# Performance work log

Hardware: AMD Instinct MI355X
Metric: run time of the kernel (lower is better)

Reference implementation:

```python
import jax, jax.numpy as jnp
import numpy as np

# ---- architecture constants (from init_kwargs / arch_args) ----
IN_BITS, IN_FRAC, BITS_PER_STREAM = 8, 4, 2
N_STREAMS = IN_BITS // BITS_PER_STREAM          # 4
W_BITS, BITS_PER_SLICE = 8, 2
N_SLICES = W_BITS // BITS_PER_SLICE             # 4
ADC_BITS = 5
ADC_MAX = 2.0 ** ADC_BITS - 1.0                 # 31
SUBARRAY_SIZE = 128
IC, OC, K, STRIDE, PAD = 64, 64, 3, 1, 1
F_TOTAL = IC * K * K                            # 576 unfolded features
N_SUB = (F_TOTAL + SUBARRAY_SIZE - 1) // SUBARRAY_SIZE  # 5 subarrays
CHUNK = -(-F_TOTAL // N_SUB)                    # 116, matches torch.chunk sizes


def bit_stream(x):
    """VectorizedInputBitStreaming.forward: fixed-point quantize + two's complement + bit-serial split."""
    int_bits = IN_BITS - IN_FRAC - 1
    max_val = 2.0 ** int_bits - 2.0 ** (-IN_FRAC)
    q = jnp.round(jnp.clip(x, -(2.0 ** int_bits), max_val) * (2 ** IN_FRAC)).astype(jnp.int32)
    q = jnp.where(q < 0, (1 << IN_BITS) + q, q)  # two's complement encode
    shifts = jnp.arange(0, IN_BITS, BITS_PER_STREAM, dtype=jnp.int32)
    return ((q[..., None] >> shifts) & ((1 << BITS_PER_STREAM) - 1)).astype(jnp.float32)


def bit_slice(w):
    """VectorizedWeightBitSlicing.forward: pos/neg split, normalize by max abs, integer bit-slice."""
    wp = jnp.maximum(w, 0.0)
    wn = jnp.maximum(-w, 0.0)
    max_abs = jnp.maximum(wp.max(), wn.max())
    max_abs = jnp.where(max_abs > 0, max_abs, 1.0)
    mv = 2 ** W_BITS - 1
    pi = jnp.round(wp / max_abs * mv).astype(jnp.int32)
    ni = jnp.round(wn / max_abs * mv).astype(jnp.int32)
    shifts = jnp.arange(0, W_BITS, BITS_PER_SLICE, dtype=jnp.int32)
    mask = (1 << BITS_PER_SLICE) - 1
    pos = ((pi[..., None] >> shifts) & mask).astype(jnp.float32)
    neg = ((ni[..., None] >> shifts) & mask).astype(jnp.float32)
    return pos, neg, max_abs


def adc(x):
    """Nbit_ADC simulated: uniform round + clip to [0, 2^adc_bits - 1]."""
    return jnp.clip(jnp.round(x), 0.0, ADC_MAX)


def _forward(inputs, weight):
    # unfold -> (B, IC*K*K, H', W') with (c, kh, kw)-major feature ordering like F.unfold
    patches = jax.lax.conv_general_dilated_patches(
        inputs, (K, K), (STRIDE, STRIDE), [(PAD, PAD), (PAD, PAD)])
    B, F, H, W = patches.shape
    P = H * W
    patches = patches.reshape(B, F, P)

    streams = bit_stream(patches)                     # (B, F, P, S)
    pos_sl, neg_sl, norm = bit_slice(weight)
    pos_m = pos_sl.reshape(OC, F, N_SLICES)           # (O, F, T)
    neg_m = neg_sl.reshape(OC, F, N_SLICES)

    # zero-pad feature dim to N_SUB*CHUNK and reshape into subarray chunks
    pad = N_SUB * CHUNK - F
    streams = jnp.pad(streams, ((0, 0), (0, pad), (0, 0), (0, 0))).reshape(B, N_SUB, CHUNK, P, N_STREAMS)
    pos_m = jnp.pad(pos_m, ((0, 0), (0, pad), (0, 0))).reshape(OC, N_SUB, CHUNK, N_SLICES)
    neg_m = jnp.pad(neg_m, ((0, 0), (0, pad), (0, 0))).reshape(OC, N_SUB, CHUNK, N_SLICES)

    # per-subarray analog MAC: (c, b, o, p, s, t)
    pos_r = jnp.einsum('bcfps,ocft->cbopst', streams, pos_m)
    neg_r = jnp.einsum('bcfps,ocft->cbopst', streams, neg_m)

    # ADC quantize, then weight by 2^(stream*bits) * 2^(slice*bits), sum over s,t and subarrays c
    scale = (2.0 ** (jnp.arange(N_STREAMS) * BITS_PER_STREAM))[:, None] * \
            (2.0 ** (jnp.arange(N_SLICES) * BITS_PER_SLICE))[None, :]
    diff = jnp.einsum('cbopst,st->bop', adc(pos_r) - adc(neg_r), scale)

    out = diff * norm / (2.0 ** IN_BITS - 1.0)
    return out.reshape(B, OC, H, W), jnp.float32(0.0)


def setup_inputs() -> dict:
    key = jax.random.key(0)
    k1, k2 = jax.random.split(key)
    inputs = jax.random.normal(k1, (4, IC, 32, 32), dtype=jnp.float32)
    # kaiming_normal_-like init
    weight = jax.random.normal(k2, (OC, IC, K, K), dtype=jnp.float32) * (2.0 / (IC * K * K)) ** 0.5
    return {"inputs": inputs, "weight": weight}


def reference(inputs, weight):
    return _forward(inputs, weight)
```

## Files before the change

### kernel.cpp

```cpp
#include <hip/hip_runtime.h>
#include <stdint.h>


typedef int v4i __attribute__((ext_vector_type(4)));
typedef unsigned int v4u __attribute__((ext_vector_type(4)));

#define WS_PART   0
#define WS_AQ     1024
#define N_PART    144

__device__ __forceinline__ unsigned char quant_in(float x) {
  x = fminf(fmaxf(x, -8.0f), 7.9375f);
  int q = (int)rintf(x * 16.0f);
  return (unsigned char)(q & 255);
}

__global__ __launch_bounds__(256) void k_prep(
    const float* __restrict__ in, const float* __restrict__ w,
    unsigned char* __restrict__ Aq, float* __restrict__ part,
    float* __restrict__ out_scalar)
{
  int bid = blockIdx.x, tid = threadIdx.x;
  if (bid == 0 && tid == 0) out_scalar[0] = 0.0f;
  if (bid < 2560) {
    unsigned int widx = bid * 256 + tid;
    unsigned int m  = ((widx >> 5) * 52429u) >> 18;
    unsigned int kw = widx - m * 160;
    int b = m >> 10, p = m & 1023;
    int y = p >> 5, x = p & 31;
    unsigned int pack = 0;
    #pragma unroll
    for (int i = 0; i < 4; ++i) {
      unsigned int k = kw * 4 + i;
      unsigned int c = k >> 7;
      unsigned int j = k & 127;
      unsigned int csize = (c == 4) ? 112 : 116;
      unsigned int bv = 0;
      if (j < csize) {
        unsigned int f  = c * 116 + j;
        unsigned int ic = (f * 7282u) >> 16;
        unsigned int r9 = f - ic * 9;
        unsigned int dy = (r9 * 11u) >> 5;
        unsigned int dx = r9 - dy * 3;
        int iy = y + (int)dy - 1, ix = x + (int)dx - 1;
        if (iy >= 0 && iy < 32 && ix >= 0 && ix < 32)
          bv = quant_in(in[((b * 64 + ic) * 32 + iy) * 32 + ix]);
      }
      pack |= bv << (8 * i);
    }
    ((unsigned int*)Aq)[widx] = pack;
  } else {
    int t = (bid - 2560) * 256 + tid;
    const float4 wv = ((const float4*)w)[t];
    float a = fmaxf(fmaxf(fabsf(wv.x), fabsf(wv.y)),
                    fmaxf(fabsf(wv.z), fabsf(wv.w)));
    #pragma unroll
    for (int off = 32; off > 0; off >>= 1)
      a = fmaxf(a, __shfl_down(a, off, 64));
    if ((tid & 63) == 0)
      part[(bid - 2560) * 4 + (tid >> 6)] = a;
  }
}

__device__ __forceinline__ v4i bits2(v4u w, int s) {
  v4u r = (w >> (unsigned)(2 * s)) & 0x03030303u;
  return (v4i)r;
}

#define BROW 656

__global__ __launch_bounds__(256) void k_main(
    const unsigned char* __restrict__ Aq, const float* __restrict__ w,
    const float* __restrict__ part, float* __restrict__ out)
{
  __shared__ unsigned char Bl[2][16][BROW];
  __shared__ float s_norm;

  int tid   = threadIdx.x;
  int lane  = tid & 63;
  int wave  = tid >> 6;
  int mtile = blockIdx.x >> 2;
  int otile = blockIdx.x & 3;

  #pragma unroll
  for (int i = 0; i < 21; ++i) {
    int d = i * 256 + tid;
    if (d < 2 * 16 * BROW / 4) ((unsigned int*)Bl)[d] = 0u;
  }
  if (wave == 0) {
    float a = part[lane];
    a = fmaxf(a, part[lane + 64]);
    if (lane < 16) a = fmaxf(a, part[lane + 128]);
    #pragma unroll
    for (int off = 32; off > 0; off >>= 1)
      a = fmaxf(a, __shfl_down(a, off, 64));
    if (lane == 0) s_norm = (a > 0.0f) ? a : 1.0f;
  }
  __syncthreads();

  float norm = s_norm;
  float sc = 255.0f / norm;
  #pragma unroll
  for (int it = 0; it < 36; ++it) {
    int idx = it * 256 + tid;
    unsigned int ol = (((unsigned)idx >> 6) * 7282u) >> 16;
    unsigned int f  = idx - ol * 576;
    float wv = w[(otile * 16 + ol) * 576 + f];
    unsigned int c = (f * 565u) >> 16;
    unsigned int j = f - c * 116;
    int kpos = c * 128 + j;
    Bl[0][ol][kpos] = (unsigned char)(int)rintf(fmaxf(wv, 0.0f) * sc);
    Bl[1][ol][kpos] = (unsigned char)(int)rintf(fmaxf(-wv, 0.0f) * sc);
  }
  __syncthreads();

  int r16  = lane & 15;
  int kgrp = lane >> 4;
  int m = mtile * 64 + wave * 16 + r16;
  const unsigned char* ap = Aq + m * 640 + kgrp * 16;
  const unsigned char* bp = &Bl[0][r16][kgrp * 16];
  const unsigned char* bn = &Bl[1][r16][kgrp * 16];

  v4i outacc = {0, 0, 0, 0};

  #pragma unroll
  for (int c = 0; c < 5; ++c) {
    v4u a0 = *(const v4u*)(ap + c * 128);
    v4u a1 = *(const v4u*)(ap + c * 128 + 64);
    v4u p0 = *(const v4u*)(bp + c * 128);
    v4u p1 = *(const v4u*)(bp + c * 128 + 64);
    v4u n0 = *(const v4u*)(bn + c * 128);
    v4u n1 = *(const v4u*)(bn + c * 128 + 64);

    v4i btp0[4], btp1[4], btn0[4], btn1[4];
    #pragma unroll
    for (int t = 0; t < 4; ++t) {
      btp0[t] = bits2(p0, t); btp1[t] = bits2(p1, t);
      btn0[t] = bits2(n0, t); btn1[t] = bits2(n1, t);
    }

    #pragma unroll
    for (int s = 0; s < 4; ++s) {
      v4i as0 = bits2(a0, s), as1 = bits2(a1, s);
      #pragma unroll
      for (int t = 0; t < 4; ++t) {
        v4i z = {0, 0, 0, 0};
        v4i pacc = __builtin_amdgcn_mfma_i32_16x16x64_i8(as0, btp0[t], z, 0, 0, 0);
        pacc     = __builtin_amdgcn_mfma_i32_16x16x64_i8(as1, btp1[t], pacc, 0, 0, 0);
        v4i nacc = __builtin_amdgcn_mfma_i32_16x16x64_i8(as0, btn0[t], z, 0, 0, 0);
        nacc     = __builtin_amdgcn_mfma_i32_16x16x64_i8(as1, btn1[t], nacc, 0, 0, 0);
        int sh = 2 * (s + t);
        #pragma unroll
        for (int r = 0; r < 4; ++r) {
          int d = (pacc[r] < 31 ? pacc[r] : 31) - (nacc[r] < 31 ? nacc[r] : 31);
          outacc[r] += d << sh;
        }
      }
    }
  }

  float fsc = norm / 255.0f;
  int oc = otile * 16 + r16;
  #pragma unroll
  for (int r = 0; r < 4; ++r) {
    int mo = mtile * 64 + wave * 16 + kgrp * 4 + r;
    int b = mo >> 10, p = mo & 1023;
    out[(b * 64 + oc) * 1024 + p] = (float)outacc[r] * fsc;
  }
}

extern "C" void kernel_launch(void* const* d_in, const int* in_sizes, int n_in,
                              void* d_out, int out_size, void* d_ws, size_t ws_size,
                              hipStream_t stream) {
  const float* inp = (const float*)d_in[0];
  const float* wgt = (const float*)d_in[1];
  float* out = (float*)d_out;
  unsigned char* ws = (unsigned char*)d_ws;

  float*         part = (float*)(ws + WS_PART);
  unsigned char* Aq   = ws + WS_AQ;

  k_prep<<<2596, 256, 0, stream>>>(inp, wgt, Aq, part, out + 262144);
  k_main<<<256, 256, 0, stream>>>(Aq, wgt, part, out);
}
```

Baseline: 79.58 us.

## Fuse input quantization, weight max-reduce and MFMA into a single kernel

Merges the prep and main kernels into one launch. Each block quantizes its own 32-row patch tile into LDS, recomputes the global weight abs-max itself, and packs the weights with float4 loads. This removes the second launch and the global round trip of the quantized patch matrix. In exchange every block redundantly reads all the weights for the max, patch rows that straddle tiles are quantized more than once, and the tile shape changes to 32 pixels by 32 output channels, with MFMA operands swapped so stores go along the pixel dimension.

```diff
diff --git a/kernel.cpp b/kernel.cpp
--- a/kernel.cpp
+++ b/kernel.cpp
@@ -5,121 +5,127 @@
 typedef int v4i __attribute__((ext_vector_type(4)));
 typedef unsigned int v4u __attribute__((ext_vector_type(4)));
 
-#define WS_PART   0
-#define WS_AQ     1024
-#define N_PART    144
-
-__device__ __forceinline__ unsigned char quant_in(float x) {
-  x = fminf(fmaxf(x, -8.0f), 7.9375f);
-  int q = (int)rintf(x * 16.0f);
-  return (unsigned char)(q & 255);
-}
-
-__global__ __launch_bounds__(256) void k_prep(
-    const float* __restrict__ in, const float* __restrict__ w,
-    unsigned char* __restrict__ Aq, float* __restrict__ part,
-    float* __restrict__ out_scalar)
-{
-  int bid = blockIdx.x, tid = threadIdx.x;
-  if (bid == 0 && tid == 0) out_scalar[0] = 0.0f;
-  if (bid < 2560) {
-    unsigned int widx = bid * 256 + tid;
-    unsigned int m  = ((widx >> 5) * 52429u) >> 18;
-    unsigned int kw = widx - m * 160;
-    int b = m >> 10, p = m & 1023;
-    int y = p >> 5, x = p & 31;
-    unsigned int pack = 0;
-    #pragma unroll
-    for (int i = 0; i < 4; ++i) {
-      unsigned int k = kw * 4 + i;
-      unsigned int c = k >> 7;
-      unsigned int j = k & 127;
-      unsigned int csize = (c == 4) ? 112 : 116;
-      unsigned int bv = 0;
-      if (j < csize) {
-        unsigned int f  = c * 116 + j;
-        unsigned int ic = (f * 7282u) >> 16;
-        unsigned int r9 = f - ic * 9;
-        unsigned int dy = (r9 * 11u) >> 5;
-        unsigned int dx = r9 - dy * 3;
-        int iy = y + (int)dy - 1, ix = x + (int)dx - 1;
-        if (iy >= 0 && iy < 32 && ix >= 0 && ix < 32)
-          bv = quant_in(in[((b * 64 + ic) * 32 + iy) * 32 + ix]);
-      }
-      pack |= bv << (8 * i);
-    }
-    ((unsigned int*)Aq)[widx] = pack;
-  } else {
-    int t = (bid - 2560) * 256 + tid;
-    const float4 wv = ((const float4*)w)[t];
-    float a = fmaxf(fmaxf(fabsf(wv.x), fabsf(wv.y)),
-                    fmaxf(fabsf(wv.z), fabsf(wv.w)));
-    #pragma unroll
-    for (int off = 32; off > 0; off >>= 1)
-      a = fmaxf(a, __shfl_down(a, off, 64));
-    if ((tid & 63) == 0)
-      part[(bid - 2560) * 4 + (tid >> 6)] = a;
-  }
-}
+#define BROW 656
 
 __device__ __forceinline__ v4i bits2(v4u w, int s) {
   v4u r = (w >> (unsigned)(2 * s)) & 0x03030303u;
   return (v4i)r;
 }
 
-#define BROW 656
+__global__ __launch_bounds__(256) void k_fused(
+    const float* __restrict__ in, const float* __restrict__ w,
+    float* __restrict__ out)
+{
+  __shared__ unsigned char Al[32 * BROW];
+  __shared__ unsigned char Bl[64 * BROW];
+  __shared__ float s_part[4];
 
-__global__ __launch_bounds__(256) void k_main(
-    const unsigned char* __restrict__ Aq, const float* __restrict__ w,
-    const float* __restrict__ part, float* __restrict__ out)
-{
-  __shared__ unsigned char Bl[2][16][BROW];
-  __shared__ float s_norm;
+  int tid = threadIdx.x;
+  int bid = blockIdx.x;
+  if (bid == 0 && tid == 0) out[262144] = 0.0f;
 
-  int tid   = threadIdx.x;
-  int lane  = tid & 63;
-  int wave  = tid >> 6;
-  int mtile = blockIdx.x >> 2;
-  int otile = blockIdx.x & 3;
+  int mtile = bid >> 1;
+  int ohalf = bid & 1;
 
   #pragma unroll
-  for (int i = 0; i < 21; ++i) {
-    int d = i * 256 + tid;
-    if (d < 2 * 16 * BROW / 4) ((unsigned int*)Bl)[d] = 0u;
+  for (int i = 0; i < 5; ++i) {
+    int idx = i * 256 + tid;
+    int loc = idx >> 2, dw = idx & 3;
+    int sign = loc >= 160 ? 1 : 0;
+    int r = loc - sign * 160;
+    unsigned int o_l = ((unsigned)r * 52429u) >> 18;
+    int c = r - (int)o_l * 5;
+    ((unsigned int*)Bl)[(sign * 32 + (int)o_l) * 164 + c * 32 + 28 + dw] = 0u;
   }
-  if (wave == 0) {
-    float a = part[lane];
-    a = fmaxf(a, part[lane + 64]);
-    if (lane < 16) a = fmaxf(a, part[lane + 128]);
+
+  {
+    int b = mtile >> 5;
+    int pbase = (mtile & 31) * 32;
+    #pragma unroll 2
+    for (int i = 0; i < 20; ++i) {
+      int d = i * 256 + tid;
+      unsigned int m_l = ((unsigned)d * 52429u) >> 23;
+      int kw = d - (int)m_l * 160;
+      int p = pbase + (int)m_l;
+      int y = p >> 5, x = p & 31;
+      unsigned int pack = 0;
+      #pragma unroll
+      for (int q = 0; q < 4; ++q) {
+        int k = kw * 4 + q;
+        int c = k >> 7, j = k & 127;
+        int csize = (c == 4) ? 112 : 116;
+        unsigned int bv = 0;
+        if (j < csize) {
+          unsigned int f  = c * 116 + j;
+          unsigned int ic = (f * 7282u) >> 16;
+          unsigned int r9 = f - ic * 9u;
+          unsigned int dy = (r9 * 11u) >> 5;
+          unsigned int dx = r9 - dy * 3u;
+          int iy = y + (int)dy - 1, ix = x + (int)dx - 1;
+          if (iy >= 0 && iy < 32 && ix >= 0 && ix < 32) {
+            float xv = in[((b * 64 + (int)ic) * 32 + iy) * 32 + ix];
+            xv = fminf(fmaxf(xv, -8.0f), 7.9375f);
+            bv = (unsigned int)((int)rintf(xv * 16.0f) & 255);
+          }
+        }
+        pack |= bv << (8 * q);
+      }
+      ((unsigned int*)Al)[(int)m_l * 164 + kw] = pack;
+    }
+  }
+
+  {
+    const float4* w4 = (const float4*)w;
+    float a = 0.0f;
+    #pragma unroll 4
+    for (int i = 0; i < 36; ++i) {
+      float4 v = w4[i * 256 + tid];
+      a = fmaxf(a, fmaxf(fmaxf(fabsf(v.x), fabsf(v.y)),
+                         fmaxf(fabsf(v.z), fabsf(v.w))));
+    }
     #pragma unroll
     for (int off = 32; off > 0; off >>= 1)
       a = fmaxf(a, __shfl_down(a, off, 64));
-    if (lane == 0) s_norm = (a > 0.0f) ? a : 1.0f;
+    if ((tid & 63) == 0) s_part[tid >> 6] = a;
   }
   __syncthreads();
 
-  float norm = s_norm;
+  float norm = fmaxf(fmaxf(s_part[0], s_part[1]), fmaxf(s_part[2], s_part[3]));
+  if (!(norm > 0.0f)) norm = 1.0f;
   float sc = 255.0f / norm;
-  #pragma unroll
-  for (int it = 0; it < 36; ++it) {
-    int idx = it * 256 + tid;
-    unsigned int ol = (((unsigned)idx >> 6) * 7282u) >> 16;
-    unsigned int f  = idx - ol * 576;
-    float wv = w[(otile * 16 + ol) * 576 + f];
-    unsigned int c = (f * 565u) >> 16;
-    unsigned int j = f - c * 116;
-    int kpos = c * 128 + j;
-    Bl[0][ol][kpos] = (unsigned char)(int)rintf(fmaxf(wv, 0.0f) * sc);
-    Bl[1][ol][kpos] = (unsigned char)(int)rintf(fmaxf(-wv, 0.0f) * sc);
+
+  #pragma unroll 2
+  for (int i = 0; i < 18; ++i) {
+    int idx = i * 256 + tid;
+    unsigned int o_l = (((unsigned)idx >> 4) * 7282u) >> 16;
+    int g = idx - (int)o_l * 144;
+    int c, jg;
+    if (g < 116) { c = (g * 565) >> 14; jg = (g - c * 29) * 4; }
+    else         { c = 4;               jg = (g - 116) * 4; }
+    int f = c * 116 + jg;
+    float4 wv = *(const float4*)(w + (ohalf * 32 + (int)o_l) * 576 + f);
+    float vv[4] = {wv.x, wv.y, wv.z, wv.w};
+    unsigned int pd = 0, nd = 0;
+    #pragma unroll
+    for (int q = 0; q < 4; ++q) {
+      unsigned int pb = (unsigned int)(int)rintf(fmaxf(vv[q], 0.0f) * sc);
+      unsigned int nb = (unsigned int)(int)rintf(fmaxf(-vv[q], 0.0f) * sc);
+      pd |= pb << (8 * q);
+      nd |= nb << (8 * q);
+    }
+    int dwo = c * 32 + (jg >> 2);
+    ((unsigned int*)Bl)[((int)o_l) * 164 + dwo]       = pd;
+    ((unsigned int*)Bl)[(32 + (int)o_l) * 164 + dwo]  = nd;
   }
   __syncthreads();
 
-  int r16  = lane & 15;
-  int kgrp = lane >> 4;
-  int m = mtile * 64 + wave * 16 + r16;
-  const unsigned char* ap = Aq + m * 640 + kgrp * 16;
-  const unsigned char* bp = &Bl[0][r16][kgrp * 16];
-  const unsigned char* bn = &Bl[1][r16][kgrp * 16];
+  int lane = tid & 63, wave = tid >> 6;
+  int msub = wave >> 1, osub = wave & 1;
+  int r16 = lane & 15, kgrp = lane >> 4;
+
+  const unsigned char* ap = Al + (msub * 16 + r16) * BROW + kgrp * 16;
+  const unsigned char* bp = Bl + (osub * 16 + r16) * BROW + kgrp * 16;
+  const unsigned char* bn = Bl + (32 + osub * 16 + r16) * BROW + kgrp * 16;
 
   v4i outacc = {0, 0, 0, 0};
 
@@ -145,10 +151,10 @@
       #pragma unroll
       for (int t = 0; t < 4; ++t) {
         v4i z = {0, 0, 0, 0};
-        v4i pacc = __builtin_amdgcn_mfma_i32_16x16x64_i8(as0, btp0[t], z, 0, 0, 0);
-        pacc     = __builtin_amdgcn_mfma_i32_16x16x64_i8(as1, btp1[t], pacc, 0, 0, 0);
-        v4i nacc = __builtin_amdgcn_mfma_i32_16x16x64_i8(as0, btn0[t], z, 0, 0, 0);
-        nacc     = __builtin_amdgcn_mfma_i32_16x16x64_i8(as1, btn1[t], nacc, 0, 0, 0);
+        v4i pacc = __builtin_amdgcn_mfma_i32_16x16x64_i8(btp0[t], as0, z, 0, 0, 0);
+        pacc     = __builtin_amdgcn_mfma_i32_16x16x64_i8(btp1[t], as1, pacc, 0, 0, 0);
+        v4i nacc = __builtin_amdgcn_mfma_i32_16x16x64_i8(btn0[t], as0, z, 0, 0, 0);
+        nacc     = __builtin_amdgcn_mfma_i32_16x16x64_i8(btn1[t], as1, nacc, 0, 0, 0);
         int sh = 2 * (s + t);
         #pragma unroll
         for (int r = 0; r < 4; ++r) {
@@ -160,13 +166,12 @@
   }
 
   float fsc = norm / 255.0f;
-  int oc = otile * 16 + r16;
+  int m = mtile * 32 + msub * 16 + r16;
+  int b = m >> 10, p = m & 1023;
+  int oc = ohalf * 32 + osub * 16 + kgrp * 4;
   #pragma unroll
-  for (int r = 0; r < 4; ++r) {
-    int mo = mtile * 64 + wave * 16 + kgrp * 4 + r;
-    int b = mo >> 10, p = mo & 1023;
-    out[(b * 64 + oc) * 1024 + p] = (float)outacc[r] * fsc;
-  }
+  for (int r = 0; r < 4; ++r)
+    out[(b * 64 + oc + r) * 1024 + p] = (float)outacc[r] * fsc;
 }
 
 extern "C" void kernel_launch(void* const* d_in, const int* in_sizes, int n_in,
@@ -175,11 +180,6 @@
   const float* inp = (const float*)d_in[0];
   const float* wgt = (const float*)d_in[1];
   float* out = (float*)d_out;
-  unsigned char* ws = (unsigned char*)d_ws;
-
-  float*         part = (float*)(ws + WS_PART);
-  unsigned char* Aq   = ws + WS_AQ;
-
-  k_prep<<<2596, 256, 0, stream>>>(inp, wgt, Aq, part, out + 262144);
-  k_main<<<256, 256, 0, stream>>>(Aq, wgt, part, out);
+  (void)d_ws; (void)ws_size;
+  k_fused<<<256, 256, 0, stream>>>(inp, wgt, out);
 }
```

Result: slower. 88.62 us (+11.4%).
